# Kernel tuning notes

Hardware: AMD Instinct MI355X
Metric: run time of the kernel (lower is better)

The kernel has to match this reference:

```python
import jax, jax.numpy as jnp
import numpy as np

F32 = jnp.float32

def denorm_px(pts, H, W):
    # kornia denormalize_pixel_coordinates: [-1,1] -> pixel
    x = (pts[..., 0] + 1.0) * (W - 1) * 0.5
    y = (pts[..., 1] + 1.0) * (H - 1) * 0.5
    return jnp.stack([x, y], axis=-1)

def norm_px(pts, H, W):
    x = pts[..., 0] * 2.0 / (W - 1) - 1.0
    y = pts[..., 1] * 2.0 / (H - 1) - 1.0
    return jnp.stack([x, y], axis=-1)

def conv2d_same(x, k, mode):
    # depthwise 2d conv, 'same' output, border via jnp.pad mode
    kh, kw = k.shape
    ph, pw = kh // 2, kw // 2
    xp = jnp.pad(x, ((0, 0), (0, 0), (ph, ph), (pw, pw)), mode=mode)
    C = x.shape[1]
    kern = jnp.broadcast_to(k[None, None], (C, 1, kh, kw)).astype(x.dtype)
    return jax.lax.conv_general_dilated(xp, kern, (1, 1), 'VALID',
        dimension_numbers=('NCHW', 'OIHW', 'NCHW'), feature_group_count=C)

def nms2d(x, k=5):
    p = k // 2
    m = jax.lax.reduce_window(x, -jnp.inf, jax.lax.max, (1, 1, k, k), (1, 1, 1, 1),
                              [(0, 0), (0, 0), (p, p), (p, p)])
    return jnp.where(x == m, x, 0.0)

def gaussian_kernel2d(ksize=7, sigma=1.0):
    ax = jnp.arange(ksize, dtype=F32) - (ksize - 1) / 2.0
    g = jnp.exp(-0.5 * (ax / sigma) ** 2)
    g = g / g.sum()
    return jnp.outer(g, g)

def gftt_response(gray):
    # kornia CornerGFTT: normalized sobel grads, blurred structure tensor, min-eig
    sx = jnp.array([[-1, 0, 1], [-2, 0, 2], [-1, 0, 1]], F32) / 8.0
    gx = conv2d_same(gray, sx, 'edge')
    gy = conv2d_same(gray, sx.T, 'edge')
    g = gaussian_kernel2d(7, 1.0)
    dx2 = conv2d_same(gx * gx, g, 'reflect')
    dy2 = conv2d_same(gy * gy, g, 'reflect')
    dxy = conv2d_same(gx * gy, g, 'reflect')
    tr = dx2 + dy2
    disc = jnp.sqrt(jnp.clip((dx2 - dy2) ** 2 + 4.0 * dxy ** 2, 0.0))
    return 0.5 * (tr - disc)

def laplacian5(x):
    k = jnp.ones((5, 5), F32).at[2, 2].set(1.0 - 25.0)
    k = k / jnp.abs(k).sum()  # kornia normalized laplacian kernel
    return conv2d_same(x, k, 'reflect')

def pairwise_project(pts, depths, poses, K):
    # pts [B,N,2] normalized; poses [B,4,4] cam-to-world
    # returns proj [B(dst),B(src),N,2] normalized + vis [B,B,N]
    B, N, _ = pts.shape
    H, W = depths.shape[-2:]
    px = denorm_px(pts, H, W)
    xi = jnp.clip(jnp.round(px[..., 0]), 0, W - 1).astype(jnp.int32)
    yi = jnp.clip(jnp.round(px[..., 1]), 0, H - 1).astype(jnp.int32)
    d = depths[jnp.arange(B)[:, None], 0, yi, xi]  # [B,N]
    Kinv = jnp.linalg.inv(K)
    hom = jnp.concatenate([px, jnp.ones_like(px[..., :1])], axis=-1)
    cam = (hom @ Kinv.T) * d[..., None]  # [B,N,3]
    R, t = poses[:, :3, :3], poses[:, :3, 3]
    world = jnp.einsum('bij,bnj->bni', R, cam) + t[:, None]
    diff = world[None] - t[:, None, None]  # [i,j,n,3]
    cam2 = jnp.einsum('iab,ijna->ijnb', R, diff)  # R_i^T (world - t_i)
    uvw = cam2 @ K.T
    z = uvw[..., 2]
    zs = jnp.where(jnp.abs(z) > 1e-6, z, 1e-6)
    u, v = uvw[..., 0] / zs, uvw[..., 1] / zs
    vis = (z > 0.1) & (u >= 0) & (u <= W - 1) & (v >= 0) & (v <= H - 1)
    return norm_px(jnp.stack([u, v], -1), H, W), vis

def pairwise_cosine_inter(x, y, eps=1e-8):
    xx = jnp.sum(x * x, -1)
    yy = jnp.sum(y * y, -1)
    xy = jnp.einsum('amd,bnd->abmn', x, y)
    den = jnp.sqrt(jnp.clip(xx[:, None, :, None] * yy[None, :, None, :], eps * eps))
    return xy / den

def pairwise_cosine_intra(x, y, eps=1e-8):
    xx = jnp.sum(x * x, -1)
    yy = jnp.sum(y * y, -1)
    xy = jnp.einsum('bmd,bnd->bmn', x, y)
    den = jnp.sqrt(jnp.clip(xx[..., :, None] * yy[..., None, :], eps * eps))
    return xy / den

def distinction_loss(desc):
    return jnp.maximum(pairwise_cosine_intra(desc, desc), 0.0).mean()

def match_loss(desc, points, proj, vis, H, W, radius=1.0):
    B, N, _ = points.shape
    src = denorm_px(jax.lax.stop_gradient(points), H, W)  # [b,m,2]
    dst = denorm_px(jax.lax.stop_gradient(proj), H, W)  # [a,b,n,2]
    x2 = jnp.sum(src * src, -1)  # [b,m]
    y2 = jnp.sum(dst * dst, -1)  # [a,b,n]
    xy = jnp.einsum('bmd,abnd->abmn', src, dst)
    dist = jnp.sqrt(jnp.clip(x2[None, :, :, None] + y2[:, :, None, :] - 2.0 * xy, 0.0))
    valid = vis[:, :, :, None]  # torch: dist[invis rows] = nan -> excluded from both masks
    tri = jnp.triu(jnp.ones((N, N), bool), 1)
    pcos = pairwise_cosine_inter(desc, desc)
    mpos = (dist <= radius) & tri & valid
    mneg = (dist > radius) & tri & valid
    pos_mean = jnp.sum(jnp.where(mpos, pcos, 0.0)) / jnp.maximum(mpos.sum(), 1)
    neg_mean = jnp.sum(jnp.where(mneg, pcos, 0.0)) / jnp.maximum(mneg.sum(), 1)
    return 1.0 - pos_mean + neg_mean

def get_corner_target(imgs, depths, poses, K, num_corners=500, radius=8):
    B, _, H, W = imgs.shape
    gray = 0.299 * imgs[:, 0:1] + 0.587 * imgs[:, 1:2] + 0.114 * imgs[:, 2:3]
    corners = nms2d(gftt_response(gray), 5)
    # MaxPool(8, return_indices) + MaxUnpool(8): keep only per-8x8-block max
    xr = corners.reshape(B, 1, H // radius, radius, W // radius, radius)
    bm = xr.max(axis=(3, 5), keepdims=True)
    keep = jnp.where(xr == bm, xr, 0.0).reshape(B, 1, H, W)
    values, idx = jax.lax.top_k(keep.reshape(B, -1), num_corners)  # [B,Nc]
    coords = jnp.stack([idx % W, idx // W], axis=2).astype(F32)  # (x,y)
    coords = norm_px(coords, H, W)
    proj, vis = pairwise_project(coords, depths, poses, K)  # [B,B,Nc,2]
    proj = jnp.where(vis[..., None], proj, -2.0)
    comb = jnp.transpose(proj, (1, 0, 2, 3)).reshape(B, B * num_corners, 2)
    px = jnp.round(denorm_px(comb, H, W)).astype(jnp.int32)
    wf = px[..., 0].reshape(-1)
    hf = px[..., 1].reshape(-1)
    bf = jnp.repeat(jnp.arange(B), B * num_corners)
    vals = jnp.tile(values.reshape(-1), B)
    mask = (wf >= 0) & (hf >= 0) & (wf < W) & (hf < H)
    vals = jnp.where(mask, vals, 0.0)
    wf = jnp.clip(wf, 0, W - 1)
    hf = jnp.clip(hf, 0, H - 1)
    target = jnp.zeros_like(corners).at[bf, 0, hf, wf].max(vals)
    target = nms2d(target, 5)
    return jax.lax.stop_gradient((target > 0).astype(F32))

def score_loss(scores, imgs, depths, poses, K):
    target = get_corner_target(imgs, depths, poses, K)
    p = jnp.clip(scores, 1e-12, 1.0 - 1e-12)
    bce = -(target * jnp.log(p) + (1.0 - target) * jnp.log(1.0 - p)).mean()
    lap = laplacian5(scores)
    return bce + (scores * jnp.exp(-lap)).mean() * 10.0

def featurenet_loss(descriptors, points, pointness, depths_dense, poses, K, imgs):
    beta = (1.0, 0.5, 1.0)
    H, W = pointness.shape[2], pointness.shape[3]
    distinction = distinction_loss(descriptors)
    cornerness = score_loss(pointness, imgs, depths_dense, poses, K)
    proj_pts, vis = pairwise_project(points, depths_dense, poses, K)
    match = match_loss(descriptors, points, proj_pts, vis, H, W, radius=1.0)
    return beta[0] * distinction + beta[1] * cornerness + beta[2] * match

def setup_inputs() -> dict:
    key = jax.random.key(0)
    ks = jax.random.split(key, 6)
    B, N, D, H, W = 6, 1024, 128, 320, 320
    descriptors = jax.random.normal(ks[0], (B, N, D), F32)
    points = jax.random.uniform(ks[1], (B, N, 2), F32, -0.9, 0.9)
    pointness = jax.random.uniform(ks[2], (B, 1, H, W), F32, 1e-3, 1.0 - 1e-3)
    depths_dense = jax.random.uniform(ks[3], (B, 1, H, W), F32, 1.0, 6.0)
    t = jax.random.uniform(ks[4], (B, 3), F32, -0.2, 0.2)
    poses = jnp.tile(jnp.eye(4, dtype=F32), (B, 1, 1)).at[:, :3, 3].set(t)
    K = jnp.array([[float(W), 0.0, W / 2.0], [0.0, float(W), H / 2.0], [0.0, 0.0, 1.0]], F32)
    imgs = jax.random.uniform(ks[5], (B, 3, H, W), F32)
    return dict(descriptors=descriptors, points=points, pointness=pointness,
                depths_dense=depths_dense, poses=poses, K=K, imgs=imgs)

def reference(descriptors, points, pointness, depths_dense, poses, K, imgs):
    return featurenet_loss(descriptors, points, pointness, depths_dense, poses, K, imgs)
```

## Files before the change

### kernel.cpp

```cpp
#include <hip/hip_runtime.h>
#include <stdint.h>

#define BB 6
#define NPTS 1024
#define DD 128
#define HH 320
#define WW 320
#define NC 500
#define HWsz (HH*WW)
#define CAP 2048
#define NBLK ((HH/8)*(WW/8))
#define TX 32
#define TY 8
#define NSLOT 64

typedef __attribute__((ext_vector_type(8))) short bf16x8;
typedef __attribute__((ext_vector_type(4))) float f32x4;

__device__ __forceinline__ int clampi(int v, int lo, int hi){ return v<lo?lo:(v>hi?hi:v); }
__device__ __forceinline__ int refl(int p, int L){ if(p<0)p=-p; if(p>=L)p=2*L-2-p; return p; }

__device__ __forceinline__ float wave_sum(float v){
  #pragma unroll
  for (int o = 32; o > 0; o >>= 1) v += __shfl_xor(v, o, 64);
  return v;
}
__device__ __forceinline__ double wave_sumd(double v){
  #pragma unroll
  for (int o = 32; o > 0; o >>= 1) v += __shfl_xor(v, o, 64);
  return v;
}
__device__ __forceinline__ float wave_max(float v){
  #pragma unroll
  for (int o = 32; o > 0; o >>= 1) v = fmaxf(v, __shfl_xor(v, o, 64));
  return v;
}

__device__ __constant__ float GW[7] = {
  0.0044330481f, 0.0540055850f, 0.2420362300f, 0.3990502700f,
  0.2420362300f, 0.0540055850f, 0.0044330481f };

struct Proj { float u, v; int vis; };

__device__ Proj project_point(float ptx, float pty, int jsrc, int itgt,
                              const float* __restrict__ depths,
                              const float* __restrict__ poses,
                              const float* __restrict__ Km)
{
  float pxx = ((ptx + 1.0f)*(float)(WW-1))*0.5f;
  float pxy = ((pty + 1.0f)*(float)(HH-1))*0.5f;
  float rx = rintf(pxx), ry = rintf(pxy);
  rx = fminf(fmaxf(rx, 0.f), (float)(WW-1));
  ry = fminf(fmaxf(ry, 0.f), (float)(HH-1));
  int xi = (int)rx, yi = (int)ry;
  float d = depths[(size_t)jsrc*HWsz + yi*WW + xi];
  float a00=Km[0],a01=Km[1],a02=Km[2],a10=Km[3],a11=Km[4],a12=Km[5],a20=Km[6],a21=Km[7],a22=Km[8];
  float det = a00*(a11*a22 - a12*a21) - a01*(a10*a22 - a12*a20) + a02*(a10*a21 - a11*a20);
  float id_ = 1.0f/det;
  float i00 = (a11*a22 - a12*a21)*id_;
  float i01 = (a02*a21 - a01*a22)*id_;
  float i02 = (a01*a12 - a02*a11)*id_;
  float i10 = (a12*a20 - a10*a22)*id_;
  float i11 = (a00*a22 - a02*a20)*id_;
  float i12 = (a02*a10 - a00*a12)*id_;
  float i20 = (a10*a21 - a11*a20)*id_;
  float i21 = (a01*a20 - a00*a21)*id_;
  float i22 = (a00*a11 - a01*a10)*id_;
  float c0 = (i00*pxx + i01*pxy + i02)*d;
  float c1 = (i10*pxx + i11*pxy + i12)*d;
  float c2 = (i20*pxx + i21*pxy + i22)*d;
  const float* Pj = poses + (size_t)jsrc*16;
  float w0 = Pj[0]*c0 + Pj[1]*c1 + Pj[2]*c2  + Pj[3];
  float w1 = Pj[4]*c0 + Pj[5]*c1 + Pj[6]*c2  + Pj[7];
  float w2 = Pj[8]*c0 + Pj[9]*c1 + Pj[10]*c2 + Pj[11];
  const float* Pi = poses + (size_t)itgt*16;
  float dx = w0 - Pi[3], dy = w1 - Pi[7], dz = w2 - Pi[11];
  float e0 = Pi[0]*dx + Pi[4]*dy + Pi[8]*dz;
  float e1 = Pi[1]*dx + Pi[5]*dy + Pi[9]*dz;
  float e2 = Pi[2]*dx + Pi[6]*dy + Pi[10]*dz;
  float uu = a00*e0 + a01*e1 + a02*e2;
  float vv = a10*e0 + a11*e1 + a12*e2;
  float zz = a20*e0 + a21*e1 + a22*e2;
  float zs = (fabsf(zz) > 1e-6f) ? zz : 1e-6f;
  Proj r;
  r.u = uu/zs; r.v = vv/zs;
  r.vis = (zz > 0.1f) && (r.u >= 0.f) && (r.u <= (float)(WW-1)) && (r.v >= 0.f) && (r.v <= (float)(HH-1));
  return r;
}

__global__ void k_gray(const float* __restrict__ imgs, float* __restrict__ gray){
  int t = blockIdx.x*blockDim.x + threadIdx.x;
  if (t >= BB*HWsz) return;
  int b = t / HWsz, p = t - b*HWsz;
  const float* base = imgs + (size_t)b*3*HWsz;
  gray[t] = 0.299f*base[p] + 0.587f*base[HWsz+p] + 0.114f*base[2*HWsz+p];
}

__global__ void k_sobel(const float* __restrict__ gray, float* __restrict__ gxx,
                        float* __restrict__ gyy, float* __restrict__ gxy){
  int t = blockIdx.x*blockDim.x + threadIdx.x;
  if (t >= BB*HWsz) return;
  int b = t / HWsz, p = t - b*HWsz;
  int y = p / WW, x = p - y*WW;
  const float* g = gray + (size_t)b*HWsz;
  int ym = clampi(y-1,0,HH-1), yp = clampi(y+1,0,HH-1);
  int xm = clampi(x-1,0,WW-1), xp = clampi(x+1,0,WW-1);
  float g00 = g[ym*WW+xm], g01 = g[ym*WW+x], g02 = g[ym*WW+xp];
  float g10 = g[y*WW+xm],                    g12 = g[y*WW+xp];
  float g20 = g[yp*WW+xm], g21 = g[yp*WW+x], g22 = g[yp*WW+xp];
  float gx = 0.125f*(g02-g00) + 0.25f*(g12-g10) + 0.125f*(g22-g20);
  float gy = 0.125f*(g20-g00) + 0.25f*(g21-g01) + 0.125f*(g22-g02);
  gxx[t] = gx*gx; gyy[t] = gy*gy; gxy[t] = gx*gy;
}

__global__ __launch_bounds__(256) void k_gauss_resp(const float* __restrict__ gxx,
        const float* __restrict__ gyy, const float* __restrict__ gxy, float* __restrict__ resp){
  __shared__ float lxx[TY+6][TX+6], lyy[TY+6][TX+6], lxy[TY+6][TX+6];
  int b = blockIdx.z;
  int x0 = blockIdx.x*TX, y0 = blockIdx.y*TY;
  const float* axx = gxx + (size_t)b*HWsz;
  const float* ayy = gyy + (size_t)b*HWsz;
  const float* axy = gxy + (size_t)b*HWsz;
  const int W2 = TX+6, H2 = TY+6;
  for (int i = threadIdx.x; i < H2*W2; i += 256){
    int ly = i / W2, lx = i - ly*W2;
    int gy = refl(y0 - 3 + ly, HH), gx = refl(x0 - 3 + lx, WW);
    size_t off = (size_t)gy*WW + gx;
    lxx[ly][lx] = axx[off]; lyy[ly][lx] = ayy[off]; lxy[ly][lx] = axy[off];
  }
  __syncthreads();
  int tx = threadIdx.x & (TX-1), ty = threadIdx.x / TX;
  float sxx=0.f, syy=0.f, sxy=0.f;
  #pragma unroll
  for (int i=0;i<7;++i){
    float wr = GW[i];
    #pragma unroll
    for (int j=0;j<7;++j){
      float wc = wr*GW[j];
      sxx += wc*lxx[ty+i][tx+j];
      syy += wc*lyy[ty+i][tx+j];
      sxy += wc*lxy[ty+i][tx+j];
    }
  }
  float tr = sxx+syy, df = sxx-syy;
  float disc = sqrtf(fmaxf(df*df + 4.f*sxy*sxy, 0.f));
  resp[(size_t)b*HWsz + (size_t)(y0+ty)*WW + (x0+tx)] = 0.5f*(tr - disc);
}

__global__ __launch_bounds__(256) void k_nms5(const float* __restrict__ resp, float* __restrict__ keep){
  __shared__ float lr[TY+4][TX+4];
  int b = blockIdx.z;
  int x0 = blockIdx.x*TX, y0 = blockIdx.y*TY;
  const float* rb = resp + (size_t)b*HWsz;
  const int W2 = TX+4, H2 = TY+4;
  for (int i = threadIdx.x; i < H2*W2; i += 256){
    int ly = i / W2, lx = i - ly*W2;
    int gy = y0 - 2 + ly, gx = x0 - 2 + lx;
    lr[ly][lx] = (gy >= 0 && gy < HH && gx >= 0 && gx < WW) ? rb[(size_t)gy*WW + gx] : -1e30f;
  }
  __syncthreads();
  int tx = threadIdx.x & (TX-1), ty = threadIdx.x / TX;
  float m = -1e30f;
  #pragma unroll
  for (int dy=0; dy<5; ++dy)
    #pragma unroll
    for (int dx=0; dx<5; ++dx) m = fmaxf(m, lr[ty+dy][tx+dx]);
  float r = lr[ty+2][tx+2];
  keep[(size_t)b*HWsz + (size_t)(y0+ty)*WW + (x0+tx)] = (r == m) ? r : 0.f;
}

__global__ void k_blockmax_compact(const float* __restrict__ keep,
        unsigned long long* __restrict__ ckeys, unsigned int* __restrict__ ccnt){
  int gw = (blockIdx.x*(int)blockDim.x + (int)threadIdx.x) >> 6;
  int lane = threadIdx.x & 63;
  if (gw >= BB*NBLK) return;
  int b = gw / NBLK; int r = gw - b*NBLK;
  int by = r / (WW/8), bx = r - by*(WW/8);
  int yy = by*8 + (lane >> 3), xx2 = bx*8 + (lane & 7);
  float v = keep[(size_t)b*HWsz + (size_t)yy*WW + xx2];
  float bm = wave_max(v);
  if (!(bm > 0.f)) return;
  unsigned long long mask = __ballot(v == bm);
  if (v == bm){
    unsigned long long key =
      ((unsigned long long)__float_as_uint(bm) << 32) |
      (unsigned long long)(0xFFFFFFFFu - (unsigned int)(yy*WW + xx2));
    int rank = __popcll(mask & ((1ull << lane) - 1ull));
    if (rank == 0){
      ckeys[(size_t)b*CAP + r] = key;
    } else {
      unsigned int slot = NBLK + atomicAdd(&ccnt[b], 1u);
      if (slot < CAP) ckeys[(size_t)b*CAP + slot] = key;
    }
  }
}

__global__ __launch_bounds__(1024) void k_top500(const unsigned long long* __restrict__ ckeys,
        float* __restrict__ cpts, float* __restrict__ cvals){
  __shared__ unsigned long long sk[CAP];
  int b = blockIdx.x;
  int tid = threadIdx.x;
  for (int i = tid; i < CAP; i += 1024)
    sk[i] = ckeys[(size_t)b*CAP + i];
  __syncthreads();
  for (int k = 2; k <= CAP; k <<= 1){
    for (int j = k >> 1; j > 0; j >>= 1){
      for (int i = tid; i < CAP; i += 1024){
        int l = i ^ j;
        if (l > i){
          unsigned long long A = sk[i], Bv = sk[l];
          bool up = ((i & k) == 0);
          if ((A > Bv) == up){ sk[i] = Bv; sk[l] = A; }
        }
      }
      __syncthreads();
    }
  }
  if (tid < NC){
    unsigned long long key = sk[CAP-1-tid];
    float val = __uint_as_float((unsigned int)(key >> 32));
    size_t o = (size_t)b*NC + tid;
    if (val > 0.f){
      unsigned int idx = 0xFFFFFFFFu - (unsigned int)(key & 0xFFFFFFFFull);
      float fx = (float)(idx % WW), fy = (float)(idx / WW);
      cpts[o*2+0] = (fx*2.0f)/(float)(WW-1) - 1.0f;
      cpts[o*2+1] = (fy*2.0f)/(float)(HH-1) - 1.0f;
      cvals[o] = val;
    } else {
      cpts[o*2+0] = __int_as_float(0x7fc00000);
      cpts[o*2+1] = __int_as_float(0x7fc00000);
      cvals[o] = 0.f;
    }
  }
}

__global__ void k_corner_scatter(const float* __restrict__ cpts, const float* __restrict__ cvals,
        const float* __restrict__ depths, const float* __restrict__ poses,
        const float* __restrict__ Km, unsigned int* __restrict__ target){
  int t = blockIdx.x*blockDim.x + threadIdx.x;
  if (t >= BB*BB*NC) return;
  int i = t / (BB*NC); int r = t - i*(BB*NC); int j = r / NC; int n = r - j*NC;
  float val = cvals[(size_t)i*NC + n];
  float ptx = cpts[((size_t)j*NC+n)*2+0];
  float pty = cpts[((size_t)j*NC+n)*2+1];
  if (!(val > 0.f) || ptx != ptx) return;
  Proj pr = project_point(ptx, pty, j, i, depths, poses, Km);
  if (!pr.vis) return;
  float nu = (pr.u*2.0f)/(float)(WW-1) - 1.0f;
  float nv = (pr.v*2.0f)/(float)(HH-1) - 1.0f;
  float px2 = ((nu+1.0f)*(float)(WW-1))*0.5f;
  float py2 = ((nv+1.0f)*(float)(HH-1))*0.5f;
  float rx = rintf(px2), ry = rintf(py2);
  if (!(rx >= 0.f && ry >= 0.f && rx <= (float)(WW-1) && ry <= (float)(HH-1))) return;
  int wf = (int)rx, hf = (int)ry;
  atomicMax(&target[(size_t)j*HWsz + hf*WW + wf], __float_as_uint(val));
}

__global__ __launch_bounds__(256) void k_score_reduce(const float* __restrict__ target,
        const float* __restrict__ scores, double* __restrict__ accs){
  __shared__ float ltg[TY+4][TX+4], lsc[TY+4][TX+4];
  __shared__ float rbuf[4][2];
  int b = blockIdx.z;
  int x0 = blockIdx.x*TX, y0 = blockIdx.y*TY;
  const float* tg = target + (size_t)b*HWsz;
  const float* sb = scores + (size_t)b*HWsz;
  const int W2 = TX+4, H2 = TY+4;
  for (int i = threadIdx.x; i < H2*W2; i += 256){
    int ly = i / W2, lx = i - ly*W2;
    int gy = y0 - 2 + ly, gx = x0 - 2 + lx;
    ltg[ly][lx] = (gy >= 0 && gy < HH && gx >= 0 && gx < WW) ? tg[(size_t)gy*WW + gx] : -1e30f;
    lsc[ly][lx] = sb[(size_t)refl(gy,HH)*WW + refl(gx,WW)];
  }
  __syncthreads();
  int tx = threadIdx.x & (TX-1), ty = threadIdx.x / TX;
  float m = -1e30f, S5 = 0.f;
  #pragma unroll
  for (int dy=0; dy<5; ++dy)
    #pragma unroll
    for (int dx=0; dx<5; ++dx){
      m = fmaxf(m, ltg[ty+dy][tx+dx]);
      S5 += lsc[ty+dy][tx+dx];
    }
  float tv = ltg[ty+2][tx+2];
  float sc = lsc[ty+2][tx+2];
  float tb = (tv > 0.f && tv == m) ? 1.f : 0.f;
  float pc = fminf(fmaxf(sc, 1e-12f), 1.0f - 1e-12f);
  float bce = -(tb*logf(pc) + (1.f-tb)*logf(1.f-pc));
  float lap = (S5 - sc)*(1.0f/48.0f) - 0.5f*sc;
  float extra = sc*expf(-lap);
  bce = wave_sum(bce); extra = wave_sum(extra);
  int wave = threadIdx.x >> 6, lane = threadIdx.x & 63;
  if (lane == 0){ rbuf[wave][0] = bce; rbuf[wave][1] = extra; }
  __syncthreads();
  if (threadIdx.x == 0){
    int slot = (blockIdx.x + blockIdx.y*(WW/TX) + blockIdx.z*400) & (NSLOT-1);
    atomicAdd(&accs[(1*NSLOT + slot)*8], (double)(rbuf[0][0]+rbuf[1][0]+rbuf[2][0]+rbuf[3][0]));
    atomicAdd(&accs[(2*NSLOT + slot)*8], (double)(rbuf[0][1]+rbuf[1][1]+rbuf[2][1]+rbuf[3][1]));
  }
}

__global__ void k_rownorm_bf16(const float* __restrict__ desc, float* __restrict__ xx,
                               unsigned short* __restrict__ dbf){
  int t = blockIdx.x*blockDim.x + threadIdx.x;
  if (t >= BB*NPTS) return;
  const float* dptr = desc + (size_t)t*DD;
  unsigned short* optr = dbf + (size_t)t*DD;
  float s = 0.f;
  for (int d = 0; d < DD; d += 4){
    float4 v = *(const float4*)(dptr + d);
    s += v.x*v.x + v.y*v.y + v.z*v.z + v.w*v.w;
    unsigned int u0 = __float_as_uint(v.x); optr[d+0] = (unsigned short)((u0 + 0x7fffu + ((u0>>16)&1u)) >> 16);
    unsigned int u1 = __float_as_uint(v.y); optr[d+1] = (unsigned short)((u1 + 0x7fffu + ((u1>>16)&1u)) >> 16);
    unsigned int u2 = __float_as_uint(v.z); optr[d+2] = (unsigned short)((u2 + 0x7fffu + ((u2>>16)&1u)) >> 16);
    unsigned int u3 = __float_as_uint(v.w); optr[d+3] = (unsigned short)((u3 + 0x7fffu + ((u3>>16)&1u)) >> 16);
  }
  xx[t] = s;
}

__global__ void k_proj_points(const float* __restrict__ points, const float* __restrict__ depths,
        const float* __restrict__ poses, const float* __restrict__ Km,
        float* __restrict__ mproj, unsigned char* __restrict__ mvis){
  int t = blockIdx.x*blockDim.x + threadIdx.x;
  if (t >= BB*BB*NPTS) return;
  int i = t / (BB*NPTS); int r = t - i*(BB*NPTS); int j = r / NPTS; int n = r - j*NPTS;
  float ptx = points[((size_t)j*NPTS+n)*2+0];
  float pty = points[((size_t)j*NPTS+n)*2+1];
  Proj pr = project_point(ptx, pty, j, i, depths, poses, Km);
  mproj[(size_t)t*2+0] = (pr.u*2.0f)/(float)(WW-1) - 1.0f;
  mproj[(size_t)t*2+1] = (pr.v*2.0f)/(float)(HH-1) - 1.0f;
  mvis[t] = pr.vis ? 1 : 0;
}

__global__ __launch_bounds__(256) void k_distinction_mfma(const unsigned short* __restrict__ dbf,
        const float* __restrict__ xx, double* __restrict__ accs){
  __shared__ float rbuf[4];
  int b = blockIdx.z;
  int tid = threadIdx.x;
  int wave = tid >> 6, lane = tid & 63;
  int wr = blockIdx.x*64 + (wave&1)*32;
  int wc = blockIdx.y*64 + (wave>>1)*32;
  int r = lane & 15, kg = lane >> 4;
  const unsigned short* descb = dbf + (size_t)b*NPTS*DD;
  const float* xb = xx + (size_t)b*NPTS;
  f32x4 c00 = {}, c01 = {}, c10 = {}, c11 = {};
  #pragma unroll
  for (int ks = 0; ks < 4; ++ks){
    int ko = ks*32 + kg*8;
    bf16x8 a0 = *(const bf16x8*)(descb + (size_t)(wr+r)*DD + ko);
    bf16x8 a1 = *(const bf16x8*)(descb + (size_t)(wr+16+r)*DD + ko);
    bf16x8 b0 = *(const bf16x8*)(descb + (size_t)(wc+r)*DD + ko);
    bf16x8 b1 = *(const bf16x8*)(descb + (size_t)(wc+16+r)*DD + ko);
    c00 = __builtin_amdgcn_mfma_f32_16x16x32_bf16(a0, b0, c00, 0, 0, 0);
    c01 = __builtin_amdgcn_mfma_f32_16x16x32_bf16(a0, b1, c01, 0, 0, 0);
    c10 = __builtin_amdgcn_mfma_f32_16x16x32_bf16(a1, b0, c10, 0, 0, 0);
    c11 = __builtin_amdgcn_mfma_f32_16x16x32_bf16(a1, b1, c11, 0, 0, 0);
  }
  float xn0 = xb[wc + r], xn1 = xb[wc + 16 + r];
  float local = 0.f;
  #pragma unroll
  for (int mi = 0; mi < 2; ++mi){
    #pragma unroll
    for (int j = 0; j < 4; ++j){
      float xm = xb[wr + mi*16 + 4*kg + j];
      float v0 = (mi ? c10[j] : c00[j]);
      float v1 = (mi ? c11[j] : c01[j]);
      local += fmaxf(v0 / sqrtf(fmaxf(xm*xn0, 1e-16f)), 0.f);
      local += fmaxf(v1 / sqrtf(fmaxf(xm*xn1, 1e-16f)), 0.f);
    }
  }
  local = wave_sum(local);
  if (lane == 0) rbuf[wave] = local;
  __syncthreads();
  if (tid == 0){
    int slot = (blockIdx.x + blockIdx.y*16 + blockIdx.z*32) & (NSLOT-1);
    atomicAdd(&accs[(0*NSLOT + slot)*8], (double)(rbuf[0]+rbuf[1]+rbuf[2]+rbuf[3]));
  }
}

__global__ __launch_bounds__(256) void k_match_mfma(const unsigned short* __restrict__ dbf,
        const float* __restrict__ xx, const float* __restrict__ points,
        const float* __restrict__ mproj, const unsigned char* __restrict__ mvis,
        double* __restrict__ accs){
  __shared__ float rbuf[4][4];
  int ab = blockIdx.z; int a = ab / BB, b = ab - a*BB;
  int ti = blockIdx.x;
  int mt = 0;
  while (ti >= 16 - mt){ ti -= 16 - mt; ++mt; }
  int nt = mt + ti;
  int tid = threadIdx.x;
  int wave = tid >> 6, lane = tid & 63;
  int wr = mt*64 + (wave&1)*32;
  int wc = nt*64 + (wave>>1)*32;
  int r = lane & 15, kg = lane >> 4;
  const unsigned short* descA = dbf + (size_t)a*NPTS*DD;
  const unsigned short* descB = dbf + (size_t)b*NPTS*DD;
  const float* xxa = xx + (size_t)a*NPTS;
  const float* xxb = xx + (size_t)b*NPTS;
  const float* pts = points + (size_t)b*NPTS*2;
  const float* mp  = mproj + (((size_t)a*BB+b)*NPTS)*2;
  const unsigned char* mv = mvis + ((size_t)a*BB+b)*NPTS;
  f32x4 c00 = {}, c01 = {}, c10 = {}, c11 = {};
  #pragma unroll
  for (int ks = 0; ks < 4; ++ks){
    int ko = ks*32 + kg*8;
    bf16x8 a0 = *(const bf16x8*)(descA + (size_t)(wr+r)*DD + ko);
    bf16x8 a1 = *(const bf16x8*)(descA + (size_t)(wr+16+r)*DD + ko);
    bf16x8 b0 = *(const bf16x8*)(descB + (size_t)(wc+r)*DD + ko);
    bf16x8 b1 = *(const bf16x8*)(descB + (size_t)(wc+16+r)*DD + ko);
    c00 = __builtin_amdgcn_mfma_f32_16x16x32_bf16(a0, b0, c00, 0, 0, 0);
    c01 = __builtin_amdgcn_mfma_f32_16x16x32_bf16(a0, b1, c01, 0, 0, 0);
    c10 = __builtin_amdgcn_mfma_f32_16x16x32_bf16(a1, b0, c10, 0, 0, 0);
    c11 = __builtin_amdgcn_mfma_f32_16x16x32_bf16(a1, b1, c11, 0, 0, 0);
  }
  float nxxv[2], ndx[2], ndy[2], ny2[2];
  #pragma unroll
  for (int ni = 0; ni < 2; ++ni){
    int n = wc + ni*16 + r;
    nxxv[ni] = xxb[n];
    float qx = mp[n*2+0], qy = mp[n*2+1];
    float dx = ((qx+1.f)*(float)(WW-1))*0.5f;
    float dy = ((qy+1.f)*(float)(HH-1))*0.5f;
    ndx[ni] = dx; ndy[ni] = dy;
    ny2[ni] = dx*dx + dy*dy;
  }
  float pos = 0.f, neg = 0.f, pcf = 0.f, ncf = 0.f;
  #pragma unroll
  for (int mi = 0; mi < 2; ++mi){
    #pragma unroll
    for (int j = 0; j < 4; ++j){
      int m = wr + mi*16 + 4*kg + j;
      if (!mv[m]) continue;
      float px = pts[m*2+0], py = pts[m*2+1];
      float sx = ((px+1.f)*(float)(WW-1))*0.5f;
      float sy = ((py+1.f)*(float)(HH-1))*0.5f;
      float x2 = sx*sx + sy*sy;
      float xm = xxa[m];
      #pragma unroll
      for (int ni = 0; ni < 2; ++ni){
        int n = wc + ni*16 + r;
        if (m >= n) continue;
        float dv = (mi ? (ni ? c11[j] : c10[j]) : (ni ? c01[j] : c00[j]));
        float d2 = x2 + ny2[ni] - 2.f*(sx*ndx[ni] + sy*ndy[ni]);
        float den = sqrtf(fmaxf(xm * nxxv[ni], 1e-16f));
        float p = dv/den;
        if (d2 <= 1.0f){ pos += p; pcf += 1.f; }
        else           { neg += p; ncf += 1.f; }
      }
    }
  }
  pos = wave_sum(pos); neg = wave_sum(neg);
  pcf = wave_sum(pcf); ncf = wave_sum(ncf);
  if (lane == 0){ rbuf[wave][0] = pos; rbuf[wave][1] = neg; rbuf[wave][2] = pcf; rbuf[wave][3] = ncf; }
  __syncthreads();
  if (tid == 0){
    int slot = (blockIdx.x + blockIdx.z*8) & (NSLOT-1);
    atomicAdd(&accs[(3*NSLOT + slot)*8], (double)(rbuf[0][0]+rbuf[1][0]+rbuf[2][0]+rbuf[3][0]));
    atomicAdd(&accs[(4*NSLOT + slot)*8], (double)(rbuf[0][1]+rbuf[1][1]+rbuf[2][1]+rbuf[3][1]));
    atomicAdd(&accs[(5*NSLOT + slot)*8], (double)(rbuf[0][2]+rbuf[1][2]+rbuf[2][2]+rbuf[3][2]));
    atomicAdd(&accs[(6*NSLOT + slot)*8], (double)(rbuf[0][3]+rbuf[1][3]+rbuf[2][3]+rbuf[3][3]));
  }
}

__global__ void k_final(const double* __restrict__ accs, float* __restrict__ out){
  int lane = threadIdx.x;
  double tot[7];
  #pragma unroll
  for (int q = 0; q < 7; ++q)
    tot[q] = wave_sumd(accs[((size_t)q*NSLOT + lane)*8]);
  if (lane == 0){
    double distinction = tot[0] / (double)((long long)BB*NPTS*NPTS);
    double bce = tot[1] / (double)((long long)BB*HWsz);
    double extra = tot[2] / (double)((long long)BB*HWsz);
    double cornerness = bce + 10.0*extra;
    double pcd = tot[5] < 0.5 ? 1.0 : tot[5];
    double ncd = tot[6] < 0.5 ? 1.0 : tot[6];
    double pos_mean = tot[3] / pcd;
    double neg_mean = tot[4] / ncd;
    double match = 1.0 - pos_mean + neg_mean;
    out[0] = (float)(distinction + 0.5*cornerness + match);
  }
}

extern "C" void kernel_launch(void* const* d_in, const int* in_sizes, int n_in,
                              void* d_out, int out_size, void* d_ws, size_t ws_size,
                              hipStream_t stream) {
  (void)in_sizes; (void)n_in; (void)out_size; (void)ws_size;
  const float* desc   = (const float*)d_in[0];
  const float* points = (const float*)d_in[1];
  const float* scores = (const float*)d_in[2];
  const float* depths = (const float*)d_in[3];
  const float* poses  = (const float*)d_in[4];
  const float* Km     = (const float*)d_in[5];
  const float* imgs   = (const float*)d_in[6];
  float* out = (float*)d_out;

  const size_t S = (size_t)BB*HWsz;
  float* gray = (float*)d_ws;
  float* bx   = gray + S;
  float* by   = bx + S;
  float* bxy  = by + S;
  float* resp = gray;
  float* keep = bx;
  unsigned long long* ckeys = (unsigned long long*)(bxy + S);
  unsigned int* ccnt = (unsigned int*)(ckeys + (size_t)BB*CAP);
  double* accs = (double*)(ccnt + 8);
  float* cpts  = (float*)(accs + 7*NSLOT*8);
  float* cvals = cpts + (size_t)BB*NC*2;
  float* xx    = cvals + (size_t)BB*NC;
  float* mproj = xx + (size_t)BB*NPTS;
  unsigned char* mvis = (unsigned char*)(mproj + (size_t)BB*BB*NPTS*2);
  unsigned short* dbf = (unsigned short*)(mvis + (size_t)BB*BB*NPTS);

  const int npx = BB*HWsz;
  dim3 blk(256);
  dim3 gpx((npx + 255)/256);
  dim3 gtile(WW/TX, HH/TY, BB);

  k_gray<<<gpx, blk, 0, stream>>>(imgs, gray);
  k_sobel<<<gpx, blk, 0, stream>>>(gray, bx, by, bxy);
  k_gauss_resp<<<gtile, blk, 0, stream>>>(bx, by, bxy, resp);

  hipMemsetAsync(by, 0, S*sizeof(float), stream);
  hipMemsetAsync(ckeys, 0,
      (size_t)BB*CAP*sizeof(unsigned long long) + 8*sizeof(unsigned int) +
      (size_t)7*NSLOT*8*sizeof(double), stream);

  k_nms5<<<gtile, blk, 0, stream>>>(resp, keep);
  {
    int n = BB*NBLK*64;
    k_blockmax_compact<<<dim3((n+255)/256), blk, 0, stream>>>(keep, ckeys, ccnt);
  }
  k_top500<<<dim3(BB), dim3(1024), 0, stream>>>(ckeys, cpts, cvals);
  {
    int n = BB*BB*NC;
    k_corner_scatter<<<dim3((n+255)/256), blk, 0, stream>>>(cpts, cvals, depths, poses, Km,
                                                            (unsigned int*)by);
  }
  k_score_reduce<<<gtile, blk, 0, stream>>>(by, scores, accs);
  {
    int n = BB*NPTS;
    k_rownorm_bf16<<<dim3((n+255)/256), blk, 0, stream>>>(desc, xx, dbf);
  }
  {
    int n = BB*BB*NPTS;
    k_proj_points<<<dim3((n+255)/256), blk, 0, stream>>>(points, depths, poses, Km, mproj, mvis);
  }
  k_distinction_mfma<<<dim3(16, 16, BB), blk, 0, stream>>>(dbf, xx, accs);
  k_match_mfma<<<dim3(136, 1, BB*BB), blk, 0, stream>>>(dbf, xx, points, mproj, mvis, accs);
  k_final<<<dim3(1), dim3(64), 0, stream>>>(accs, out);
}
```

Baseline: 231.7 us.

## Fuse gray+sobel, NMS+blockmax compaction, rownorm+projection kernels; use rsqrt

Computes grayscale inside a tiled Sobel kernel using a shared-memory halo, which removes the gray intermediate buffer and one launch. Folds the 8x8 block-max compaction into the NMS kernel through a shared tile, so the keep map is never written or read back from global memory. Merges the descriptor row-norm kernel and the point-projection kernel into a single launch, and replaces divide-by-sqrt with multiply-by-rsqrt in the MFMA epilogues. This saves launches and global traffic, at the cost of recomputing gray for halo pixels and slightly different rounding from rsqrt.

```diff
diff --git a/kernel.cpp b/kernel.cpp
--- a/kernel.cpp
+++ b/kernel.cpp
@@ -88,29 +88,30 @@
   return r;
 }
 
-__global__ void k_gray(const float* __restrict__ imgs, float* __restrict__ gray){
-  int t = blockIdx.x*blockDim.x + threadIdx.x;
-  if (t >= BB*HWsz) return;
-  int b = t / HWsz, p = t - b*HWsz;
-  const float* base = imgs + (size_t)b*3*HWsz;
-  gray[t] = 0.299f*base[p] + 0.587f*base[HWsz+p] + 0.114f*base[2*HWsz+p];
-}
-
-__global__ void k_sobel(const float* __restrict__ gray, float* __restrict__ gxx,
-                        float* __restrict__ gyy, float* __restrict__ gxy){
-  int t = blockIdx.x*blockDim.x + threadIdx.x;
-  if (t >= BB*HWsz) return;
-  int b = t / HWsz, p = t - b*HWsz;
-  int y = p / WW, x = p - y*WW;
-  const float* g = gray + (size_t)b*HWsz;
-  int ym = clampi(y-1,0,HH-1), yp = clampi(y+1,0,HH-1);
-  int xm = clampi(x-1,0,WW-1), xp = clampi(x+1,0,WW-1);
-  float g00 = g[ym*WW+xm], g01 = g[ym*WW+x], g02 = g[ym*WW+xp];
-  float g10 = g[y*WW+xm],                    g12 = g[y*WW+xp];
-  float g20 = g[yp*WW+xm], g21 = g[yp*WW+x], g22 = g[yp*WW+xp];
+__global__ __launch_bounds__(256) void k_graysobel(const float* __restrict__ imgs,
+        float* __restrict__ gxx, float* __restrict__ gyy, float* __restrict__ gxy){
+  __shared__ float lg[TY+2][TX+2];
+  int b = blockIdx.z;
+  int x0 = blockIdx.x*TX, y0 = blockIdx.y*TY;
+  const float* br = imgs + (size_t)b*3*HWsz;
+  const float* bg = br + HWsz;
+  const float* bb = bg + HWsz;
+  const int W2 = TX+2, H2 = TY+2;
+  for (int i = threadIdx.x; i < H2*W2; i += 256){
+    int ly = i / W2, lx = i - ly*W2;
+    int gy = clampi(y0 - 1 + ly, 0, HH-1), gx = clampi(x0 - 1 + lx, 0, WW-1);
+    size_t off = (size_t)gy*WW + gx;
+    lg[ly][lx] = 0.299f*br[off] + 0.587f*bg[off] + 0.114f*bb[off];
+  }
+  __syncthreads();
+  int tx = threadIdx.x & (TX-1), ty = threadIdx.x / TX;
+  float g00 = lg[ty][tx],   g01 = lg[ty][tx+1],   g02 = lg[ty][tx+2];
+  float g10 = lg[ty+1][tx],                        g12 = lg[ty+1][tx+2];
+  float g20 = lg[ty+2][tx], g21 = lg[ty+2][tx+1], g22 = lg[ty+2][tx+2];
   float gx = 0.125f*(g02-g00) + 0.25f*(g12-g10) + 0.125f*(g22-g20);
   float gy = 0.125f*(g20-g00) + 0.25f*(g21-g01) + 0.125f*(g22-g02);
-  gxx[t] = gx*gx; gyy[t] = gy*gy; gxy[t] = gx*gy;
+  size_t o = (size_t)b*HWsz + (size_t)(y0+ty)*WW + (x0+tx);
+  gxx[o] = gx*gx; gyy[o] = gy*gy; gxy[o] = gx*gy;
 }
 
 __global__ __launch_bounds__(256) void k_gauss_resp(const float* __restrict__ gxx,
@@ -147,8 +148,10 @@
   resp[(size_t)b*HWsz + (size_t)(y0+ty)*WW + (x0+tx)] = 0.5f*(tr - disc);
 }
 
-__global__ __launch_bounds__(256) void k_nms5(const float* __restrict__ resp, float* __restrict__ keep){
+__global__ __launch_bounds__(256) void k_nmsblk(const float* __restrict__ resp,
+        unsigned long long* __restrict__ ckeys, unsigned int* __restrict__ ccnt){
   __shared__ float lr[TY+4][TX+4];
+  __shared__ float lk[TY][TX];
   int b = blockIdx.z;
   int x0 = blockIdx.x*TX, y0 = blockIdx.y*TY;
   const float* rb = resp + (size_t)b*HWsz;
@@ -166,28 +169,23 @@
     #pragma unroll
     for (int dx=0; dx<5; ++dx) m = fmaxf(m, lr[ty+dy][tx+dx]);
   float r = lr[ty+2][tx+2];
-  keep[(size_t)b*HWsz + (size_t)(y0+ty)*WW + (x0+tx)] = (r == m) ? r : 0.f;
-}
-
-__global__ void k_blockmax_compact(const float* __restrict__ keep,
-        unsigned long long* __restrict__ ckeys, unsigned int* __restrict__ ccnt){
-  int gw = (blockIdx.x*(int)blockDim.x + (int)threadIdx.x) >> 6;
-  int lane = threadIdx.x & 63;
-  if (gw >= BB*NBLK) return;
-  int b = gw / NBLK; int r = gw - b*NBLK;
-  int by = r / (WW/8), bx = r - by*(WW/8);
-  int yy = by*8 + (lane >> 3), xx2 = bx*8 + (lane & 7);
-  float v = keep[(size_t)b*HWsz + (size_t)yy*WW + xx2];
+  lk[ty][tx] = (r == m) ? r : 0.f;
+  __syncthreads();
+  int wave = threadIdx.x >> 6, lane = threadIdx.x & 63;
+  int ly = lane >> 3, lx = wave*8 + (lane & 7);
+  float v = lk[ly][lx];
   float bm = wave_max(v);
   if (!(bm > 0.f)) return;
   unsigned long long mask = __ballot(v == bm);
   if (v == bm){
+    int yy = y0 + ly, xx2 = x0 + lx;
     unsigned long long key =
       ((unsigned long long)__float_as_uint(bm) << 32) |
       (unsigned long long)(0xFFFFFFFFu - (unsigned int)(yy*WW + xx2));
     int rank = __popcll(mask & ((1ull << lane) - 1ull));
+    int rblk = blockIdx.y*(WW/8) + blockIdx.x*4 + wave;
     if (rank == 0){
-      ckeys[(size_t)b*CAP + r] = key;
+      ckeys[(size_t)b*CAP + rblk] = key;
     } else {
       unsigned int slot = NBLK + atomicAdd(&ccnt[b], 1u);
       if (slot < CAP) ckeys[(size_t)b*CAP + slot] = key;
@@ -299,36 +297,36 @@
   }
 }
 
-__global__ void k_rownorm_bf16(const float* __restrict__ desc, float* __restrict__ xx,
-                               unsigned short* __restrict__ dbf){
-  int t = blockIdx.x*blockDim.x + threadIdx.x;
-  if (t >= BB*NPTS) return;
-  const float* dptr = desc + (size_t)t*DD;
-  unsigned short* optr = dbf + (size_t)t*DD;
-  float s = 0.f;
-  for (int d = 0; d < DD; d += 4){
-    float4 v = *(const float4*)(dptr + d);
-    s += v.x*v.x + v.y*v.y + v.z*v.z + v.w*v.w;
-    unsigned int u0 = __float_as_uint(v.x); optr[d+0] = (unsigned short)((u0 + 0x7fffu + ((u0>>16)&1u)) >> 16);
-    unsigned int u1 = __float_as_uint(v.y); optr[d+1] = (unsigned short)((u1 + 0x7fffu + ((u1>>16)&1u)) >> 16);
-    unsigned int u2 = __float_as_uint(v.z); optr[d+2] = (unsigned short)((u2 + 0x7fffu + ((u2>>16)&1u)) >> 16);
-    unsigned int u3 = __float_as_uint(v.w); optr[d+3] = (unsigned short)((u3 + 0x7fffu + ((u3>>16)&1u)) >> 16);
-  }
-  xx[t] = s;
-}
-
-__global__ void k_proj_points(const float* __restrict__ points, const float* __restrict__ depths,
+__global__ void k_rowproj(const float* __restrict__ desc, float* __restrict__ xx,
+        unsigned short* __restrict__ dbf,
+        const float* __restrict__ points, const float* __restrict__ depths,
         const float* __restrict__ poses, const float* __restrict__ Km,
         float* __restrict__ mproj, unsigned char* __restrict__ mvis){
   int t = blockIdx.x*blockDim.x + threadIdx.x;
-  if (t >= BB*BB*NPTS) return;
-  int i = t / (BB*NPTS); int r = t - i*(BB*NPTS); int j = r / NPTS; int n = r - j*NPTS;
+  if (t < BB*NPTS){
+    const float* dptr = desc + (size_t)t*DD;
+    unsigned short* optr = dbf + (size_t)t*DD;
+    float s = 0.f;
+    for (int d = 0; d < DD; d += 4){
+      float4 v = *(const float4*)(dptr + d);
+      s += v.x*v.x + v.y*v.y + v.z*v.z + v.w*v.w;
+      unsigned int u0 = __float_as_uint(v.x); optr[d+0] = (unsigned short)((u0 + 0x7fffu + ((u0>>16)&1u)) >> 16);
+      unsigned int u1 = __float_as_uint(v.y); optr[d+1] = (unsigned short)((u1 + 0x7fffu + ((u1>>16)&1u)) >> 16);
+      unsigned int u2 = __float_as_uint(v.z); optr[d+2] = (unsigned short)((u2 + 0x7fffu + ((u2>>16)&1u)) >> 16);
+      unsigned int u3 = __float_as_uint(v.w); optr[d+3] = (unsigned short)((u3 + 0x7fffu + ((u3>>16)&1u)) >> 16);
+    }
+    xx[t] = s;
+    return;
+  }
+  int t2 = t - BB*NPTS;
+  if (t2 >= BB*BB*NPTS) return;
+  int i = t2 / (BB*NPTS); int r = t2 - i*(BB*NPTS); int j = r / NPTS; int n = r - j*NPTS;
   float ptx = points[((size_t)j*NPTS+n)*2+0];
   float pty = points[((size_t)j*NPTS+n)*2+1];
   Proj pr = project_point(ptx, pty, j, i, depths, poses, Km);
-  mproj[(size_t)t*2+0] = (pr.u*2.0f)/(float)(WW-1) - 1.0f;
-  mproj[(size_t)t*2+1] = (pr.v*2.0f)/(float)(HH-1) - 1.0f;
-  mvis[t] = pr.vis ? 1 : 0;
+  mproj[(size_t)t2*2+0] = (pr.u*2.0f)/(float)(WW-1) - 1.0f;
+  mproj[(size_t)t2*2+1] = (pr.v*2.0f)/(float)(HH-1) - 1.0f;
+  mvis[t2] = pr.vis ? 1 : 0;
 }
 
 __global__ __launch_bounds__(256) void k_distinction_mfma(const unsigned short* __restrict__ dbf,
@@ -364,8 +362,8 @@
       float xm = xb[wr + mi*16 + 4*kg + j];
       float v0 = (mi ? c10[j] : c00[j]);
       float v1 = (mi ? c11[j] : c01[j]);
-      local += fmaxf(v0 / sqrtf(fmaxf(xm*xn0, 1e-16f)), 0.f);
-      local += fmaxf(v1 / sqrtf(fmaxf(xm*xn1, 1e-16f)), 0.f);
+      local += fmaxf(v0 * rsqrtf(fmaxf(xm*xn0, 1e-16f)), 0.f);
+      local += fmaxf(v1 * rsqrtf(fmaxf(xm*xn1, 1e-16f)), 0.f);
     }
   }
   local = wave_sum(local);
@@ -441,8 +439,7 @@
         if (m >= n) continue;
         float dv = (mi ? (ni ? c11[j] : c10[j]) : (ni ? c01[j] : c00[j]));
         float d2 = x2 + ny2[ni] - 2.f*(sx*ndx[ni] + sy*ndy[ni]);
-        float den = sqrtf(fmaxf(xm * nxxv[ni], 1e-16f));
-        float p = dv/den;
+        float p = dv * rsqrtf(fmaxf(xm * nxxv[ni], 1e-16f));
         if (d2 <= 1.0f){ pos += p; pcf += 1.f; }
         else           { neg += p; ncf += 1.f; }
       }
@@ -495,13 +492,11 @@
   float* out = (float*)d_out;
 
   const size_t S = (size_t)BB*HWsz;
-  float* gray = (float*)d_ws;
-  float* bx   = gray + S;
-  float* by   = bx + S;
-  float* bxy  = by + S;
-  float* resp = gray;
-  float* keep = bx;
-  unsigned long long* ckeys = (unsigned long long*)(bxy + S);
+  float* resp = (float*)d_ws;
+  float* gxx  = resp + S;
+  float* gyy  = gxx + S;
+  float* gxy  = gyy + S;
+  unsigned long long* ckeys = (unsigned long long*)(gxy + S);
   unsigned int* ccnt = (unsigned int*)(ckeys + (size_t)BB*CAP);
   double* accs = (double*)(ccnt + 8);
   float* cpts  = (float*)(accs + 7*NSLOT*8);
@@ -511,39 +506,29 @@
   unsigned char* mvis = (unsigned char*)(mproj + (size_t)BB*BB*NPTS*2);
   unsigned short* dbf = (unsigned short*)(mvis + (size_t)BB*BB*NPTS);
 
-  const int npx = BB*HWsz;
   dim3 blk(256);
-  dim3 gpx((npx + 255)/256);
   dim3 gtile(WW/TX, HH/TY, BB);
 
-  k_gray<<<gpx, blk, 0, stream>>>(imgs, gray);
-  k_sobel<<<gpx, blk, 0, stream>>>(gray, bx, by, bxy);
-  k_gauss_resp<<<gtile, blk, 0, stream>>>(bx, by, bxy, resp);
-
-  hipMemsetAsync(by, 0, S*sizeof(float), stream);
+  k_graysobel<<<gtile, blk, 0, stream>>>(imgs, gxx, gyy, gxy);
+  k_gauss_resp<<<gtile, blk, 0, stream>>>(gxx, gyy, gxy, resp);
+
+  hipMemsetAsync(gyy, 0, S*sizeof(float), stream);
   hipMemsetAsync(ckeys, 0,
       (size_t)BB*CAP*sizeof(unsigned long long) + 8*sizeof(unsigned int) +
       (size_t)7*NSLOT*8*sizeof(double), stream);
 
-  k_nms5<<<gtile, blk, 0, stream>>>(resp, keep);
-  {
-    int n = BB*NBLK*64;
-    k_blockmax_compact<<<dim3((n+255)/256), blk, 0, stream>>>(keep, ckeys, ccnt);
-  }
+  k_nmsblk<<<gtile, blk, 0, stream>>>(resp, ckeys, ccnt);
   k_top500<<<dim3(BB), dim3(1024), 0, stream>>>(ckeys, cpts, cvals);
   {
     int n = BB*BB*NC;
     k_corner_scatter<<<dim3((n+255)/256), blk, 0, stream>>>(cpts, cvals, depths, poses, Km,
-                                                            (unsigned int*)by);
-  }
-  k_score_reduce<<<gtile, blk, 0, stream>>>(by, scores, accs);
+                                                            (unsigned int*)gyy);
+  }
+  k_score_reduce<<<gtile, blk, 0, stream>>>(gyy, scores, accs);
   {
-    int n = BB*NPTS;
-    k_rownorm_bf16<<<dim3((n+255)/256), blk, 0, stream>>>(desc, xx, dbf);
-  }
-  {
-    int n = BB*BB*NPTS;
-    k_proj_points<<<dim3((n+255)/256), blk, 0, stream>>>(points, depths, poses, Km, mproj, mvis);
+    int n = BB*NPTS + BB*BB*NPTS;
+    k_rowproj<<<dim3((n+255)/256), blk, 0, stream>>>(desc, xx, dbf, points, depths, poses, Km,
+                                                     mproj, mvis);
   }
   k_distinction_mfma<<<dim3(16, 16, BB), blk, 0, stream>>>(dbf, xx, accs);
   k_match_mfma<<<dim3(136, 1, BB*BB), blk, 0, stream>>>(dbf, xx, points, mproj, mvis, accs);
```

Result: faster. 215.3 us (-7.1%).
